# Kernel tuning notes

Hardware: AMD Instinct MI355X
Metric: run time of the kernel (lower is better)

The kernel has to match this reference:

```python
import jax, jax.numpy as jnp
import numpy as np

B, T, D_IN, H1, H2 = 32, 2048, 1024, 512, 32


def setup_inputs() -> dict:
    key = jax.random.key(0)
    ks = jax.random.split(key, 8)
    avf_out = jax.random.normal(ks[0], (B, T, D_IN), dtype=jnp.float32)
    # seq_len in [1, T] so every sample has a non-empty slice (matches torch usage)
    seq_len = jax.random.randint(ks[1], (B,), 1, T + 1, dtype=jnp.int32)
    s = 0.02
    W1 = jax.random.normal(ks[2], (D_IN, H1), dtype=jnp.float32) * s
    b1 = jnp.zeros((H1,), dtype=jnp.float32)
    W2 = jax.random.normal(ks[3], (H1, H2), dtype=jnp.float32) * s
    b2 = jnp.zeros((H2,), dtype=jnp.float32)
    W3 = jax.random.normal(ks[4], (H2, 1), dtype=jnp.float32) * s
    b3 = jnp.zeros((1,), dtype=jnp.float32)
    return {"avf_out": avf_out, "W1": W1, "b1": b1, "W2": W2, "b2": b2,
            "W3": W3, "b3": b3, "seq_len": seq_len}


def reference(avf_out, W1, b1, W2, b2, W3, b3, seq_len):
    h = jax.nn.relu(jnp.einsum('btd,dh->bth', avf_out, W1) + b1)
    h = jnp.einsum('bth,hk->btk', h, W2) + b2
    logits = jax.nn.sigmoid(jnp.einsum('btk,ko->bto', h, W3) + b3)[..., 0]  # [B, T]
    # ragged per-sample top-k (k = seq_len//16 + 1 over first seq_len entries) + mean,
    # vectorized via masked descending sort + cumsum (no per-sample loop)
    Tn = logits.shape[1]
    valid = jnp.arange(Tn)[None, :] < seq_len[:, None]            # [B, T]
    NEG = jnp.float32(-1.0)  # below sigmoid range, so padded slots never enter top-k
    masked = jnp.where(valid, logits, NEG)
    sorted_desc = -jnp.sort(-masked, axis=1)                      # [B, T] descending
    csum = jnp.cumsum(sorted_desc, axis=1)
    k = seq_len // 16 + 1                                         # k <= seq_len always
    topk_sum = jnp.take_along_axis(csum, (k - 1)[:, None].astype(jnp.int32), axis=1)[:, 0]
    return topk_sum / k.astype(logits.dtype)                      # [B]
```

## Files before the change

kernel.cpp:

```cpp
#include <hip/hip_runtime.h>

typedef __bf16 bf16;
typedef __bf16 bf16x4 __attribute__((ext_vector_type(4)));
typedef __bf16 bf16x8 __attribute__((ext_vector_type(8)));
typedef float f32x4 __attribute__((ext_vector_type(4)));

#define K_TOT 1024
#define N_TOT 512
#define T_SEQ 2048
#define NB 32
#define M_TILE 160
#define MAX_J 13
#define NBLK_TGT 256

__device__ __forceinline__ void async16(const void* g, void* l) {
    __builtin_amdgcn_global_load_lds(
        (const __attribute__((address_space(1))) unsigned int*)g,
        (__attribute__((address_space(3))) unsigned int*)l, 16, 0, 0);
}

__global__ __launch_bounds__(256) void transpose_prep(
        const float* __restrict__ W1, bf16* __restrict__ W1T,
        const float* __restrict__ W2, const float* __restrict__ b2,
        const float* __restrict__ W3, const float* __restrict__ b3,
        const int* __restrict__ seq_len,
        float* __restrict__ v, int* __restrict__ tiles, int* __restrict__ done) {
    __shared__ float tile[32][33];
    const int t = threadIdx.x;
    const int k0 = blockIdx.x * 32;
    const int n0 = blockIdx.y * 32;
#pragma unroll
    for (int p = 0; p < 4; p++) {
        int kl = p * 8 + (t >> 5);
        int nl = t & 31;
        tile[kl][nl] = W1[(k0 + kl) * 512 + n0 + nl];
    }
    __syncthreads();
#pragma unroll
    for (int p = 0; p < 4; p++) {
        int nl = p * 8 + (t >> 5);
        int kl = t & 31;
        W1T[(n0 + nl) * 1024 + k0 + kl] = (bf16)tile[kl][nl];
    }

    if (blockIdx.x == 0 && blockIdx.y == 0) {
        __shared__ int Ls[32], nb2[32], off2[32], rbest;
        for (int h = t; h < 512; h += 256) {
            float s = 0.f;
#pragma unroll
            for (int c = 0; c < 32; c++) s += W2[h * 32 + c] * W3[c];
            v[h] = s;
        }
        if (t == 0) {
            float cc = b3[0];
            for (int c = 0; c < 32; c++) cc += b2[c] * W3[c];
            v[512] = cc;
            rbest = M_TILE;
        }
        if (t < 32) {
            Ls[t] = seq_len[t];
            done[t] = 0;
        }
        __syncthreads();
        if (t < M_TILE) {
            int R = t + 1, S = 0;
#pragma unroll 4
            for (int i = 0; i < 32; i++) S += (Ls[i] + R - 1) / R;
            if (S <= NBLK_TGT) atomicMin(&rbest, R);
        }
        __syncthreads();
        const int R = rbest;
        if (t < 32) nb2[t] = (Ls[t] + R - 1) / R;
        __syncthreads();
        if (t == 0) {
            int a = 0;
            for (int i = 0; i < 32; i++) { off2[i] = a; a += nb2[i]; }
            tiles[0] = a;
        }
        __syncthreads();
        for (int idx = t; idx < 32 * 256; idx += 256) {
            int b = idx >> 8, j = idx & 255;
            int nb = nb2[b];
            if (j < nb) {
                int L = Ls[b];
                int q = L / nb, r = L % nb;
                int start = j * q + (j < r ? j : r);
                int nrows = q + (j < r ? 1 : 0);
                tiles[1 + off2[b] + j] = (b << 19) | (start << 8) | nrows;
            }
        }
    }
}

__device__ __forceinline__ int sw_idx(int row, int e) {
    return row * 64 + (((e >> 3) ^ (row & 7)) << 3) + (e & 7);
}

__global__ __launch_bounds__(512, 2) void gemm_fused(const float* __restrict__ A,
                                                     const bf16* __restrict__ W1T,
                                                     const float* __restrict__ b1,
                                                     const float* __restrict__ v,
                                                     const int* __restrict__ tiles,
                                                     const int* __restrict__ seq_len,
                                                     int* __restrict__ done,
                                                     float* __restrict__ logits,
                                                     float* __restrict__ out) {
    __shared__ bf16 smem[M_TILE * 64 + 2 * N_TOT * 64];
    bf16* As = smem;
    bf16* Bs0 = smem + M_TILE * 64;
    bf16* Bs1 = Bs0 + N_TOT * 64;

    const int nact = tiles[0];
    if ((int)blockIdx.x >= nact) return;
    const int w = tiles[1 + blockIdx.x];
    const int bsmp = w >> 19;
    const int start = (w >> 8) & 0x7FF;
    const int mrows = w & 0xFF;
    const int m0 = bsmp * T_SEQ + start;

    const int t = threadIdx.x;
    const int wave = t >> 6, lane = t & 63;
    const int q = lane >> 4, l15 = lane & 15;
    const int wm = wave >> 2, wn = wave & 3;

    const int c16 = t & 15, r0 = t >> 4;
    bool alive[5];
    const float* agp[5];
#pragma unroll
    for (int p = 0; p < 5; p++) {
        alive[p] = (r0 + p * 32) < mrows;
        agp[p] = A + (size_t)(m0 + r0 + p * 32) * K_TOT + c16 * 4;
    }
    bool mlive[5];
#pragma unroll
    for (int p = 0; p < 5; p++) mlive[p] = (wm * 80 + p * 16) < mrows;

    const int bl_row = wave * 64 + (lane >> 3);
    const int bl_chunk = (lane & 7) ^ ((lane >> 3) & 7);
    const bf16* bgp = W1T + (size_t)bl_row * K_TOT + bl_chunk * 8;

    f32x4 acc[5][8] = {};
    float4 av[5];

    auto loadA = [&](int k0) {
#pragma unroll
        for (int p = 0; p < 5; p++)
            if (alive[p]) av[p] = *(const float4*)(agp[p] + k0);
    };
    auto asyncB = [&](int k0, bf16* bs) {
#pragma unroll
        for (int j = 0; j < 8; j++)
            async16(bgp + k0 + (size_t)j * 8 * K_TOT, bs + (wave * 64 + j * 8) * 64);
    };
    auto writeA = [&]() {
#pragma unroll
        for (int p = 0; p < 5; p++) {
            if (!alive[p]) continue;
            bf16x4 wv;
            wv[0] = (bf16)av[p].x; wv[1] = (bf16)av[p].y;
            wv[2] = (bf16)av[p].z; wv[3] = (bf16)av[p].w;
            int row = r0 + p * 32;
            int chunk = c16 >> 1;
            int idx = row * 64 + ((chunk ^ (row & 7)) << 3) + (c16 & 1) * 4;
            *(bf16x4*)(&As[idx]) = wv;
        }
    };
    auto mfma_phase = [&](const bf16* bs) {
#pragma unroll
        for (int kk = 0; kk < 64; kk += 32) {
            const int e = kk + q * 8;
            bf16x8 af[5];
#pragma unroll
            for (int mi = 0; mi < 5; mi++)
                if (mlive[mi])
                    af[mi] = *(const bf16x8*)(&As[sw_idx(wm * 80 + mi * 16 + l15, e)]);
#pragma unroll
            for (int nh = 0; nh < 8; nh += 4) {
                bf16x8 bfv[4];
#pragma unroll
                for (int ni = 0; ni < 4; ni++)
                    bfv[ni] = *(const bf16x8*)(&bs[sw_idx(wn * 128 + (nh + ni) * 16 + l15, e)]);
#pragma unroll
                for (int mi = 0; mi < 5; mi++)
                    if (mlive[mi])
#pragma unroll
                        for (int ni = 0; ni < 4; ni++)
                            acc[mi][nh + ni] = __builtin_amdgcn_mfma_f32_16x16x32_bf16(
                                af[mi], bfv[ni], acc[mi][nh + ni], 0, 0, 0);
            }
        }
    };

    loadA(0);
    asyncB(0, Bs0);
    writeA();
    __syncthreads();

#pragma unroll 1
    for (int k = 0; k < 16; k++) {
        bf16* bcur = (k & 1) ? Bs1 : Bs0;
        bf16* bnxt = (k & 1) ? Bs0 : Bs1;
        if (k < 15) {
            loadA((k + 1) * 64);
            asyncB((k + 1) * 64, bnxt);
        }
        mfma_phase(bcur);
        __syncthreads();
        if (k < 15) {
            writeA();
            __syncthreads();
        }
    }

    float bb[8], vv[8];
#pragma unroll
    for (int ni = 0; ni < 8; ni++) {
        int col = wn * 128 + ni * 16 + l15;
        bb[ni] = b1[col];
        vv[ni] = v[col];
    }
    const float cconst = v[512];

    float* part = (float*)smem;

#pragma unroll
    for (int mi = 0; mi < 5; mi++) {
#pragma unroll
        for (int r = 0; r < 4; r++) {
            float s = 0.f;
#pragma unroll
            for (int ni = 0; ni < 8; ni++)
                s += fmaxf(acc[mi][ni][r] + bb[ni], 0.f) * vv[ni];
            s += __shfl_xor(s, 1);
            s += __shfl_xor(s, 2);
            s += __shfl_xor(s, 4);
            s += __shfl_xor(s, 8);
            if (l15 == 0) {
                int row = wm * 80 + mi * 16 + q * 4 + r;
                part[row * 4 + wn] = s;
            }
        }
    }
    __syncthreads();
    if (t < mrows) {
        float s = part[t * 4] + part[t * 4 + 1] + part[t * 4 + 2] + part[t * 4 + 3] + cconst;
        logits[m0 + t] = 1.f / (1.f + __expf(-s));
    }

    const int L = seq_len[bsmp];

    float* vals  = (float*)smem;
    int*   redi  = (int*)(vals + 2048);
    unsigned* mnx = (unsigned*)(redi + 16);
    float* redf  = (float*)(mnx + 16);
    int*   wflag = (int*)(redf + 8);

    __syncthreads();
    if (t == 0) {
        __threadfence();
        int old = atomicAdd(&done[bsmp], mrows);
        int win = (old + mrows == L);
        if (win) __threadfence();
        *wflag = win;
    }
    __syncthreads();
    if (!*wflag) return;

    const int kk = (L >> 4) + 1;
    const float* p = logits + bsmp * T_SEQ;

    unsigned mn = 0x3f800000u, mx = 0u;
    for (int i = t; i < L; i += 512) {
        float x = p[i];
        vals[i] = x;
        unsigned u = __float_as_uint(x);
        mn = min(mn, u); mx = max(mx, u);
    }
#pragma unroll
    for (int m = 32; m >= 1; m >>= 1) {
        mn = min(mn, (unsigned)__shfl_xor((int)mn, m));
        mx = max(mx, (unsigned)__shfl_xor((int)mx, m));
    }
    if (lane == 0) { mnx[wave] = mn; mnx[8 + wave] = mx; }
    __syncthreads();
    unsigned lo = mnx[0], hi = mnx[8];
#pragma unroll
    for (int w8 = 1; w8 < 8; w8++) {
        lo = min(lo, mnx[w8]); hi = max(hi, mnx[8 + w8]);
    }
    __syncthreads();

    int rb = 0;
    while (lo < hi) {
        unsigned wd = hi - lo;
        unsigned t1 = wd / 3u + 1u;
        unsigned m1 = lo + t1;
        unsigned m2 = lo + (wd - wd / 3u);
        if (m2 < m1) m2 = m1;
        float f1 = __uint_as_float(m1), f2 = __uint_as_float(m2);
        int c1 = 0, c2 = 0;
        for (int i = t; i < L; i += 512) {
            float x = vals[i];
            c1 += (x >= f1) ? 1 : 0;
            c2 += (x >= f2) ? 1 : 0;
        }
        int packed = (c1 << 12) | c2;
#pragma unroll
        for (int m = 32; m >= 1; m >>= 1) packed += __shfl_xor(packed, m);
        if (lane == 0) redi[(rb & 1) * 8 + wave] = packed;
        __syncthreads();
        int tot = 0;
#pragma unroll
        for (int w8 = 0; w8 < 8; w8++) tot += redi[(rb & 1) * 8 + w8];
        int C2 = tot & 0xFFF, C1 = tot >> 12;
        if (C2 >= kk)      { lo = m2; }
        else if (C1 >= kk) { lo = m1; hi = m2 - 1; }
        else               { hi = m1 - 1; }
        rb++;
    }
    const float thr = __uint_as_float(lo);

    int cg = 0; float sg = 0.f;
    for (int i = t; i < L; i += 512) {
        float x = vals[i];
        if (x > thr) { cg += 1; sg += x; }
    }
#pragma unroll
    for (int m = 32; m >= 1; m >>= 1) {
        cg += __shfl_xor(cg, m);
        sg += __shfl_xor(sg, m);
    }
    if (lane == 0) { redi[(rb & 1) * 8 + wave] = cg; redf[wave] = sg; }
    __syncthreads();
    if (t == 0) {
        int cgt = 0; float sgt = 0.f;
#pragma unroll
        for (int w8 = 0; w8 < 8; w8++) { cgt += redi[(rb & 1) * 8 + w8]; sgt += redf[w8]; }
        out[bsmp] = (sgt + (float)(kk - cgt) * thr) / (float)kk;
    }
}

extern "C" void kernel_launch(void* const* d_in, const int* in_sizes, int n_in,
                              void* d_out, int out_size, void* d_ws, size_t ws_size,
                              hipStream_t stream) {
    const float* avf = (const float*)d_in[0];
    const float* W1  = (const float*)d_in[1];
    const float* b1  = (const float*)d_in[2];
    const float* W2  = (const float*)d_in[3];
    const float* b2  = (const float*)d_in[4];
    const float* W3  = (const float*)d_in[5];
    const float* b3  = (const float*)d_in[6];
    const int* seq_len = (const int*)d_in[7];
    float* out = (float*)d_out;

    char* ws = (char*)d_ws;
    bf16*  W1T    = (bf16*)ws;
    float* v      = (float*)(ws + (1 << 20));
    int*   tiles  = (int*)(ws + (1 << 20) + 4096);
    int*   done   = (int*)(ws + (1 << 20) + 8192);
    float* logits = (float*)(ws + (1 << 20) + 12288);

    transpose_prep<<<dim3(32, 16), 256, 0, stream>>>(W1, W1T, W2, b2, W3, b3,
                                                     seq_len, v, tiles, done);
    gemm_fused<<<NB * MAX_J, 512, 0, stream>>>(avf, W1T, b1, v, tiles, seq_len,
                                               done, logits, out);
}
```

Before: 394.7 us.

## Fuse weight transpose/prep and GEMM into one cooperative kernel with grid sync

Merges the W1 transpose/bf16 conversion and tile-schedule prep kernel into the main GEMM+top-k kernel. It launches a single cooperative grid of 256 blocks that syncs after the prep phase, then loops over tile slots. This removes one kernel launch and the inter-kernel gap, and spreads the transpose across all blocks. The cost is a grid-wide barrier and the requirement that all 256 blocks be co-resident, which cooperative launch enforces.

New measurement: 530.9 us. 34.5% more time.

```diff
diff --git a/kernel.cpp b/kernel.cpp
--- a/kernel.cpp
+++ b/kernel.cpp
@@ -1,4 +1,7 @@
 #include <hip/hip_runtime.h>
+#include <hip/hip_cooperative_groups.h>
+
+namespace cg = cooperative_groups;
 
 typedef __bf16 bf16;
 typedef __bf16 bf16x4 __attribute__((ext_vector_type(4)));
@@ -10,8 +13,7 @@
 #define T_SEQ 2048
 #define NB 32
 #define M_TILE 160
-#define MAX_J 13
-#define NBLK_TGT 256
+#define NBLK 256
 
 __device__ __forceinline__ void async16(const void* g, void* l) {
     __builtin_amdgcn_global_load_lds(
@@ -19,37 +21,55 @@
         (__attribute__((address_space(3))) unsigned int*)l, 16, 0, 0);
 }
 
-__global__ __launch_bounds__(256) void transpose_prep(
-        const float* __restrict__ W1, bf16* __restrict__ W1T,
-        const float* __restrict__ W2, const float* __restrict__ b2,
-        const float* __restrict__ W3, const float* __restrict__ b3,
-        const int* __restrict__ seq_len,
-        float* __restrict__ v, int* __restrict__ tiles, int* __restrict__ done) {
-    __shared__ float tile[32][33];
+__device__ __forceinline__ int sw_idx(int row, int e) {
+    return row * 64 + (((e >> 3) ^ (row & 7)) << 3) + (e & 7);
+}
+
+__global__ __launch_bounds__(512, 2) void fused_all(
+        const float* __restrict__ A,  const float* __restrict__ W1,
+        const float* __restrict__ b1, const float* __restrict__ W2,
+        const float* __restrict__ b2, const float* __restrict__ W3,
+        const float* __restrict__ b3, const int* __restrict__ seq_len,
+        bf16* __restrict__ W1T, float* __restrict__ v,
+        int* __restrict__ tiles, int* __restrict__ done,
+        float* __restrict__ logits, float* __restrict__ out) {
+    __shared__ bf16 smem[M_TILE * 64 + 2 * N_TOT * 64];
+    bf16* As = smem;
+    bf16* Bs0 = smem + M_TILE * 64;
+    bf16* Bs1 = Bs0 + N_TOT * 64;
+
     const int t = threadIdx.x;
-    const int k0 = blockIdx.x * 32;
-    const int n0 = blockIdx.y * 32;
-#pragma unroll
-    for (int p = 0; p < 4; p++) {
-        int kl = p * 8 + (t >> 5);
-        int nl = t & 31;
-        tile[kl][nl] = W1[(k0 + kl) * 512 + n0 + nl];
+    const int bid = blockIdx.x;
+    const int wave = t >> 6, lane = t & 63;
+    const int q = lane >> 4, l15 = lane & 15;
+    const int wm = wave >> 2, wn = wave & 3;
+
+    {
+        float* tt = (float*)smem;
+        const int k0 = (bid >> 3) * 32;
+        const int n0 = (bid & 7) * 64;
+#pragma unroll
+        for (int p = 0; p < 4; p++) {
+            int kl = p * 8 + (t >> 6);
+            int nl = t & 63;
+            tt[kl * 65 + nl] = W1[(size_t)(k0 + kl) * 512 + n0 + nl];
+        }
+        __syncthreads();
+#pragma unroll
+        for (int p = 0; p < 4; p++) {
+            int row = p * 16 + (t >> 5);
+            int col = t & 31;
+            W1T[(size_t)(n0 + row) * 1024 + k0 + col] = (bf16)tt[col * 65 + row];
+        }
     }
-    __syncthreads();
-#pragma unroll
-    for (int p = 0; p < 4; p++) {
-        int nl = p * 8 + (t >> 5);
-        int kl = t & 31;
-        W1T[(n0 + nl) * 1024 + k0 + kl] = (bf16)tile[kl][nl];
-    }
-
-    if (blockIdx.x == 0 && blockIdx.y == 0) {
-        __shared__ int Ls[32], nb2[32], off2[32], rbest;
-        for (int h = t; h < 512; h += 256) {
+
+    __shared__ int Ls[32], nb2[32], off2[32], rbest;
+    if (bid == 0) {
+        {
             float s = 0.f;
 #pragma unroll
-            for (int c = 0; c < 32; c++) s += W2[h * 32 + c] * W3[c];
-            v[h] = s;
+            for (int c = 0; c < 32; c++) s += W2[t * 32 + c] * W3[c];
+            v[t] = s;
         }
         if (t == 0) {
             float cc = b3[0];
@@ -59,14 +79,14 @@
         }
         if (t < 32) {
             Ls[t] = seq_len[t];
-            done[t] = 0;
+            atomicExch(&done[t], 0);
         }
         __syncthreads();
         if (t < M_TILE) {
             int R = t + 1, S = 0;
 #pragma unroll 4
             for (int i = 0; i < 32; i++) S += (Ls[i] + R - 1) / R;
-            if (S <= NBLK_TGT) atomicMin(&rbest, R);
+            if (S <= NBLK) atomicMin(&rbest, R);
         }
         __syncthreads();
         const int R = rbest;
@@ -78,265 +98,249 @@
             tiles[0] = a;
         }
         __syncthreads();
-        for (int idx = t; idx < 32 * 256; idx += 256) {
+        for (int idx = t; idx < 32 * 256; idx += 512) {
             int b = idx >> 8, j = idx & 255;
             int nb = nb2[b];
             if (j < nb) {
                 int L = Ls[b];
-                int q = L / nb, r = L % nb;
-                int start = j * q + (j < r ? j : r);
-                int nrows = q + (j < r ? 1 : 0);
+                int qq = L / nb, r = L % nb;
+                int start = j * qq + (j < r ? j : r);
+                int nrows = qq + (j < r ? 1 : 0);
                 tiles[1 + off2[b] + j] = (b << 19) | (start << 8) | nrows;
             }
         }
     }
-}
-
-__device__ __forceinline__ int sw_idx(int row, int e) {
-    return row * 64 + (((e >> 3) ^ (row & 7)) << 3) + (e & 7);
-}
-
-__global__ __launch_bounds__(512, 2) void gemm_fused(const float* __restrict__ A,
-                                                     const bf16* __restrict__ W1T,
-                                                     const float* __restrict__ b1,
-                                                     const float* __restrict__ v,
-                                                     const int* __restrict__ tiles,
-                                                     const int* __restrict__ seq_len,
-                                                     int* __restrict__ done,
-                                                     float* __restrict__ logits,
-                                                     float* __restrict__ out) {
-    __shared__ bf16 smem[M_TILE * 64 + 2 * N_TOT * 64];
-    bf16* As = smem;
-    bf16* Bs0 = smem + M_TILE * 64;
-    bf16* Bs1 = Bs0 + N_TOT * 64;
+
+    __threadfence();
+    cg::this_grid().sync();
+    __threadfence();
 
     const int nact = tiles[0];
-    if ((int)blockIdx.x >= nact) return;
-    const int w = tiles[1 + blockIdx.x];
-    const int bsmp = w >> 19;
-    const int start = (w >> 8) & 0x7FF;
-    const int mrows = w & 0xFF;
-    const int m0 = bsmp * T_SEQ + start;
-
-    const int t = threadIdx.x;
-    const int wave = t >> 6, lane = t & 63;
-    const int q = lane >> 4, l15 = lane & 15;
-    const int wm = wave >> 2, wn = wave & 3;
-
-    const int c16 = t & 15, r0 = t >> 4;
-    bool alive[5];
-    const float* agp[5];
-#pragma unroll
-    for (int p = 0; p < 5; p++) {
-        alive[p] = (r0 + p * 32) < mrows;
-        agp[p] = A + (size_t)(m0 + r0 + p * 32) * K_TOT + c16 * 4;
-    }
-    bool mlive[5];
-#pragma unroll
-    for (int p = 0; p < 5; p++) mlive[p] = (wm * 80 + p * 16) < mrows;
 
     const int bl_row = wave * 64 + (lane >> 3);
     const int bl_chunk = (lane & 7) ^ ((lane >> 3) & 7);
     const bf16* bgp = W1T + (size_t)bl_row * K_TOT + bl_chunk * 8;
-
-    f32x4 acc[5][8] = {};
-    float4 av[5];
-
-    auto loadA = [&](int k0) {
-#pragma unroll
-        for (int p = 0; p < 5; p++)
-            if (alive[p]) av[p] = *(const float4*)(agp[p] + k0);
-    };
-    auto asyncB = [&](int k0, bf16* bs) {
-#pragma unroll
-        for (int j = 0; j < 8; j++)
-            async16(bgp + k0 + (size_t)j * 8 * K_TOT, bs + (wave * 64 + j * 8) * 64);
-    };
-    auto writeA = [&]() {
+    const int c16 = t & 15, r0 = t >> 4;
+
+#pragma unroll 1
+    for (int slot = bid; slot < nact; slot += NBLK) {
+        __syncthreads();
+        const int w = tiles[1 + slot];
+        const int bsmp = w >> 19;
+        const int start = (w >> 8) & 0x7FF;
+        const int mrows = w & 0xFF;
+        const int m0 = bsmp * T_SEQ + start;
+
+        bool alive[5];
+        const float* agp[5];
 #pragma unroll
         for (int p = 0; p < 5; p++) {
-            if (!alive[p]) continue;
-            bf16x4 wv;
-            wv[0] = (bf16)av[p].x; wv[1] = (bf16)av[p].y;
-            wv[2] = (bf16)av[p].z; wv[3] = (bf16)av[p].w;
-            int row = r0 + p * 32;
-            int chunk = c16 >> 1;
-            int idx = row * 64 + ((chunk ^ (row & 7)) << 3) + (c16 & 1) * 4;
-            *(bf16x4*)(&As[idx]) = wv;
-        }
-    };
-    auto mfma_phase = [&](const bf16* bs) {
-#pragma unroll
-        for (int kk = 0; kk < 64; kk += 32) {
-            const int e = kk + q * 8;
-            bf16x8 af[5];
-#pragma unroll
-            for (int mi = 0; mi < 5; mi++)
-                if (mlive[mi])
-                    af[mi] = *(const bf16x8*)(&As[sw_idx(wm * 80 + mi * 16 + l15, e)]);
-#pragma unroll
-            for (int nh = 0; nh < 8; nh += 4) {
-                bf16x8 bfv[4];
-#pragma unroll
-                for (int ni = 0; ni < 4; ni++)
-                    bfv[ni] = *(const bf16x8*)(&bs[sw_idx(wn * 128 + (nh + ni) * 16 + l15, e)]);
+            alive[p] = (r0 + p * 32) < mrows;
+            agp[p] = A + (size_t)(m0 + r0 + p * 32) * K_TOT + c16 * 4;
+        }
+        bool mlive[5];
+#pragma unroll
+        for (int p = 0; p < 5; p++) mlive[p] = (wm * 80 + p * 16) < mrows;
+
+        f32x4 acc[5][8] = {};
+        float4 av[5];
+
+        auto loadA = [&](int k0) {
+#pragma unroll
+            for (int p = 0; p < 5; p++)
+                if (alive[p]) av[p] = *(const float4*)(agp[p] + k0);
+        };
+        auto asyncB = [&](int k0, bf16* bs) {
+#pragma unroll
+            for (int j = 0; j < 8; j++)
+                async16(bgp + k0 + (size_t)j * 8 * K_TOT, bs + (wave * 64 + j * 8) * 64);
+        };
+        auto writeA = [&]() {
+#pragma unroll
+            for (int p = 0; p < 5; p++) {
+                if (!alive[p]) continue;
+                bf16x4 wv;
+                wv[0] = (bf16)av[p].x; wv[1] = (bf16)av[p].y;
+                wv[2] = (bf16)av[p].z; wv[3] = (bf16)av[p].w;
+                int row = r0 + p * 32;
+                int chunk = c16 >> 1;
+                int idx = row * 64 + ((chunk ^ (row & 7)) << 3) + (c16 & 1) * 4;
+                *(bf16x4*)(&As[idx]) = wv;
+            }
+        };
+        auto mfma_phase = [&](const bf16* bs) {
+#pragma unroll
+            for (int kk = 0; kk < 64; kk += 32) {
+                const int e = kk + q * 8;
+                bf16x8 af[5];
 #pragma unroll
                 for (int mi = 0; mi < 5; mi++)
                     if (mlive[mi])
-#pragma unroll
-                        for (int ni = 0; ni < 4; ni++)
-                            acc[mi][nh + ni] = __builtin_amdgcn_mfma_f32_16x16x32_bf16(
-                                af[mi], bfv[ni], acc[mi][nh + ni], 0, 0, 0);
-            }
-        }
-    };
-
-    loadA(0);
-    asyncB(0, Bs0);
-    writeA();
-    __syncthreads();
+                        af[mi] = *(const bf16x8*)(&As[sw_idx(wm * 80 + mi * 16 + l15, e)]);
+#pragma unroll
+                for (int nh = 0; nh < 8; nh += 4) {
+                    bf16x8 bfv[4];
+#pragma unroll
+                    for (int ni = 0; ni < 4; ni++)
+                        bfv[ni] = *(const bf16x8*)(&bs[sw_idx(wn * 128 + (nh + ni) * 16 + l15, e)]);
+#pragma unroll
+                    for (int mi = 0; mi < 5; mi++)
+                        if (mlive[mi])
+#pragma unroll
+                            for (int ni = 0; ni < 4; ni++)
+                                acc[mi][nh + ni] = __builtin_amdgcn_mfma_f32_16x16x32_bf16(
+                                    af[mi], bfv[ni], acc[mi][nh + ni], 0, 0, 0);
+                }
+            }
+        };
+
+        loadA(0);
+        asyncB(0, Bs0);
+        writeA();
+        __syncthreads();
 
 #pragma unroll 1
-    for (int k = 0; k < 16; k++) {
-        bf16* bcur = (k & 1) ? Bs1 : Bs0;
-        bf16* bnxt = (k & 1) ? Bs0 : Bs1;
-        if (k < 15) {
-            loadA((k + 1) * 64);
-            asyncB((k + 1) * 64, bnxt);
-        }
-        mfma_phase(bcur);
-        __syncthreads();
-        if (k < 15) {
-            writeA();
+        for (int k = 0; k < 16; k++) {
+            bf16* bcur = (k & 1) ? Bs1 : Bs0;
+            bf16* bnxt = (k & 1) ? Bs0 : Bs1;
+            if (k < 15) {
+                loadA((k + 1) * 64);
+                asyncB((k + 1) * 64, bnxt);
+            }
+            mfma_phase(bcur);
             __syncthreads();
-        }
-    }
-
-    float bb[8], vv[8];
-#pragma unroll
-    for (int ni = 0; ni < 8; ni++) {
-        int col = wn * 128 + ni * 16 + l15;
-        bb[ni] = b1[col];
-        vv[ni] = v[col];
-    }
-    const float cconst = v[512];
-
-    float* part = (float*)smem;
-
-#pragma unroll
-    for (int mi = 0; mi < 5; mi++) {
-#pragma unroll
-        for (int r = 0; r < 4; r++) {
-            float s = 0.f;
-#pragma unroll
-            for (int ni = 0; ni < 8; ni++)
-                s += fmaxf(acc[mi][ni][r] + bb[ni], 0.f) * vv[ni];
-            s += __shfl_xor(s, 1);
-            s += __shfl_xor(s, 2);
-            s += __shfl_xor(s, 4);
-            s += __shfl_xor(s, 8);
-            if (l15 == 0) {
-                int row = wm * 80 + mi * 16 + q * 4 + r;
-                part[row * 4 + wn] = s;
-            }
-        }
-    }
-    __syncthreads();
-    if (t < mrows) {
-        float s = part[t * 4] + part[t * 4 + 1] + part[t * 4 + 2] + part[t * 4 + 3] + cconst;
-        logits[m0 + t] = 1.f / (1.f + __expf(-s));
-    }
-
-    const int L = seq_len[bsmp];
-
-    float* vals  = (float*)smem;
-    int*   redi  = (int*)(vals + 2048);
-    unsigned* mnx = (unsigned*)(redi + 16);
-    float* redf  = (float*)(mnx + 16);
-    int*   wflag = (int*)(redf + 8);
-
-    __syncthreads();
-    if (t == 0) {
-        __threadfence();
-        int old = atomicAdd(&done[bsmp], mrows);
-        int win = (old + mrows == L);
-        if (win) __threadfence();
-        *wflag = win;
-    }
-    __syncthreads();
-    if (!*wflag) return;
-
-    const int kk = (L >> 4) + 1;
-    const float* p = logits + bsmp * T_SEQ;
-
-    unsigned mn = 0x3f800000u, mx = 0u;
-    for (int i = t; i < L; i += 512) {
-        float x = p[i];
-        vals[i] = x;
-        unsigned u = __float_as_uint(x);
-        mn = min(mn, u); mx = max(mx, u);
-    }
-#pragma unroll
-    for (int m = 32; m >= 1; m >>= 1) {
-        mn = min(mn, (unsigned)__shfl_xor((int)mn, m));
-        mx = max(mx, (unsigned)__shfl_xor((int)mx, m));
-    }
-    if (lane == 0) { mnx[wave] = mn; mnx[8 + wave] = mx; }
-    __syncthreads();
-    unsigned lo = mnx[0], hi = mnx[8];
-#pragma unroll
-    for (int w8 = 1; w8 < 8; w8++) {
-        lo = min(lo, mnx[w8]); hi = max(hi, mnx[8 + w8]);
-    }
-    __syncthreads();
-
-    int rb = 0;
-    while (lo < hi) {
-        unsigned wd = hi - lo;
-        unsigned t1 = wd / 3u + 1u;
-        unsigned m1 = lo + t1;
-        unsigned m2 = lo + (wd - wd / 3u);
-        if (m2 < m1) m2 = m1;
-        float f1 = __uint_as_float(m1), f2 = __uint_as_float(m2);
-        int c1 = 0, c2 = 0;
+            if (k < 15) {
+                writeA();
+                __syncthreads();
+            }
+        }
+
+        float bb[8], vv[8];
+#pragma unroll
+        for (int ni = 0; ni < 8; ni++) {
+            int col = wn * 128 + ni * 16 + l15;
+            bb[ni] = b1[col];
+            vv[ni] = v[col];
+        }
+        const float cconst = v[512];
+
+        float* part = (float*)smem;
+
+#pragma unroll
+        for (int mi = 0; mi < 5; mi++) {
+#pragma unroll
+            for (int r = 0; r < 4; r++) {
+                float s = 0.f;
+#pragma unroll
+                for (int ni = 0; ni < 8; ni++)
+                    s += fmaxf(acc[mi][ni][r] + bb[ni], 0.f) * vv[ni];
+                s += __shfl_xor(s, 1);
+                s += __shfl_xor(s, 2);
+                s += __shfl_xor(s, 4);
+                s += __shfl_xor(s, 8);
+                if (l15 == 0) {
+                    int row = wm * 80 + mi * 16 + q * 4 + r;
+                    part[row * 4 + wn] = s;
+                }
+            }
+        }
+        __syncthreads();
+        if (t < mrows) {
+            float s = part[t * 4] + part[t * 4 + 1] + part[t * 4 + 2] + part[t * 4 + 3] + cconst;
+            logits[m0 + t] = 1.f / (1.f + __expf(-s));
+        }
+
+        const int L = seq_len[bsmp];
+
+        float* vals  = (float*)smem;
+        int*   redi  = (int*)(vals + 2048);
+        unsigned* mnx = (unsigned*)(redi + 16);
+        float* redf  = (float*)(mnx + 16);
+        int*   wflag = (int*)(redf + 8);
+
+        __syncthreads();
+        if (t == 0) {
+            __threadfence();
+            int old = atomicAdd(&done[bsmp], mrows);
+            int win = (old + mrows == L);
+            if (win) __threadfence();
+            *wflag = win;
+        }
+        __syncthreads();
+        if (!*wflag) continue;
+
+        const int kk2 = (L >> 4) + 1;
+        const float* p = logits + bsmp * T_SEQ;
+
+        unsigned mn = 0x3f800000u, mx = 0u;
+        for (int i = t; i < L; i += 512) {
+            float x = p[i];
+            vals[i] = x;
+            unsigned u = __float_as_uint(x);
+            mn = min(mn, u); mx = max(mx, u);
+        }
+#pragma unroll
+        for (int m = 32; m >= 1; m >>= 1) {
+            mn = min(mn, (unsigned)__shfl_xor((int)mn, m));
+            mx = max(mx, (unsigned)__shfl_xor((int)mx, m));
+        }
+        if (lane == 0) { mnx[wave] = mn; mnx[8 + wave] = mx; }
+        __syncthreads();
+        unsigned lo = mnx[0], hi = mnx[8];
+#pragma unroll
+        for (int w8 = 1; w8 < 8; w8++) {
+            lo = min(lo, mnx[w8]); hi = max(hi, mnx[8 + w8]);
+        }
+        __syncthreads();
+
+        int rb = 0;
+        while (lo < hi) {
+            unsigned wd = hi - lo;
+            unsigned t1 = wd / 3u + 1u;
+            unsigned m1 = lo + t1;
+            unsigned m2 = lo + (wd - wd / 3u);
+            if (m2 < m1) m2 = m1;
+            float f1 = __uint_as_float(m1), f2 = __uint_as_float(m2);
+            int c1 = 0, c2 = 0;
+            for (int i = t; i < L; i += 512) {
+                float x = vals[i];
+                c1 += (x >= f1) ? 1 : 0;
+                c2 += (x >= f2) ? 1 : 0;
+            }
+            int packed = (c1 << 12) | c2;
+#pragma unroll
+            for (int m = 32; m >= 1; m >>= 1) packed += __shfl_xor(packed, m);
+            if (lane == 0) redi[(rb & 1) * 8 + wave] = packed;
+            __syncthreads();
+            int tot = 0;
+#pragma unroll
+            for (int w8 = 0; w8 < 8; w8++) tot += redi[(rb & 1) * 8 + w8];
+            int C2 = tot & 0xFFF, C1 = tot >> 12;
+            if (C2 >= kk2)      { lo = m2; }
+            else if (C1 >= kk2) { lo = m1; hi = m2 - 1; }
+            else                { hi = m1 - 1; }
+            rb++;
+        }
+        const float thr = __uint_as_float(lo);
+
+        int cg2 = 0; float sg = 0.f;
         for (int i = t; i < L; i += 512) {
             float x = vals[i];
-            c1 += (x >= f1) ? 1 : 0;
-            c2 += (x >= f2) ? 1 : 0;
-        }
-        int packed = (c1 << 12) | c2;
-#pragma unroll
-        for (int m = 32; m >= 1; m >>= 1) packed += __shfl_xor(packed, m);
-        if (lane == 0) redi[(rb & 1) * 8 + wave] = packed;
-        __syncthreads();
-        int tot = 0;
-#pragma unroll
-        for (int w8 = 0; w8 < 8; w8++) tot += redi[(rb & 1) * 8 + w8];
-        int C2 = tot & 0xFFF, C1 = tot >> 12;
-        if (C2 >= kk)      { lo = m2; }
-        else if (C1 >= kk) { lo = m1; hi = m2 - 1; }
-        else               { hi = m1 - 1; }
-        rb++;
-    }
-    const float thr = __uint_as_float(lo);
-
-    int cg = 0; float sg = 0.f;
-    for (int i = t; i < L; i += 512) {
-        float x = vals[i];
-        if (x > thr) { cg += 1; sg += x; }
-    }
-#pragma unroll
-    for (int m = 32; m >= 1; m >>= 1) {
-        cg += __shfl_xor(cg, m);
-        sg += __shfl_xor(sg, m);
-    }
-    if (lane == 0) { redi[(rb & 1) * 8 + wave] = cg; redf[wave] = sg; }
-    __syncthreads();
-    if (t == 0) {
-        int cgt = 0; float sgt = 0.f;
-#pragma unroll
-        for (int w8 = 0; w8 < 8; w8++) { cgt += redi[(rb & 1) * 8 + w8]; sgt += redf[w8]; }
-        out[bsmp] = (sgt + (float)(kk - cgt) * thr) / (float)kk;
+            if (x > thr) { cg2 += 1; sg += x; }
+        }
+#pragma unroll
+        for (int m = 32; m >= 1; m >>= 1) {
+            cg2 += __shfl_xor(cg2, m);
+            sg  += __shfl_xor(sg, m);
+        }
+        if (lane == 0) { redi[(rb & 1) * 8 + wave] = cg2; redf[wave] = sg; }
+        __syncthreads();
+        if (t == 0) {
+            int cgt = 0; float sgt = 0.f;
+#pragma unroll
+            for (int w8 = 0; w8 < 8; w8++) { cgt += redi[(rb & 1) * 8 + w8]; sgt += redf[w8]; }
+            out[bsmp] = (sgt + (float)(kk2 - cgt) * thr) / (float)kk2;
+        }
     }
 }
 
@@ -360,8 +364,10 @@
     int*   done   = (int*)(ws + (1 << 20) + 8192);
     float* logits = (float*)(ws + (1 << 20) + 12288);
 
-    transpose_prep<<<dim3(32, 16), 256, 0, stream>>>(W1, W1T, W2, b2, W3, b3,
-                                                     seq_len, v, tiles, done);
-    gemm_fused<<<NB * MAX_J, 512, 0, stream>>>(avf, W1T, b1, v, tiles, seq_len,
-                                               done, logits, out);
+    void* args[] = {(void*)&avf, (void*)&W1, (void*)&b1, (void*)&W2,
+                    (void*)&b2, (void*)&W3, (void*)&b3, (void*)&seq_len,
+                    (void*)&W1T, (void*)&v, (void*)&tiles, (void*)&done,
+                    (void*)&logits, (void*)&out};
+    hipLaunchCooperativeKernel((const void*)fused_all, dim3(NBLK), dim3(512),
+                               args, 0, stream);
 }
```
